# Optimization experiments

Measured on AMD Instinct MI355X. Metric: run time of the kernel, lower is better.

Reference implementation:

```python
import jax, jax.numpy as jnp
import numpy as np

NUM_HEADS = 4
D_K = 64
D_MODEL = NUM_HEADS * D_K  # 256
SEN_LEN = 8192
N_GROUPS = 4096
BASE_LEN = 64
N_EDGES = N_GROUPS * BASE_LEN  # 262144
PATH_LEN = 64


def setup_inputs() -> dict:
    rng = np.random.default_rng(0)
    key = jax.random.key(0)
    ks = jax.random.split(key, 16)

    # ragged group lengths, each >= 2, summing exactly to N_EDGES
    half = N_GROUPS // 2
    r = rng.integers(-(BASE_LEN - 2), BASE_LEN - 1, size=half)
    edge_len = np.concatenate([BASE_LEN + r, BASE_LEN - r]).astype(np.int64)
    assert edge_len.sum() == N_EDGES and edge_len.min() >= 2

    # distinct token ids; include src=0 and tar=1 so path_agg branches fire
    perm = rng.permutation(np.arange(2, SEN_LEN))[: N_GROUPS - 2]
    token_ids = np.concatenate([np.array([0, 1]), perm]).astype(np.int64)

    def w(k, shape):
        return jax.random.normal(k, shape, jnp.float32) / np.sqrt(shape[-1]).astype(np.float32)

    return {
        "path": jax.random.normal(ks[0], (PATH_LEN, D_MODEL), jnp.float32),
        "path_len": PATH_LEN,
        "q": jax.random.normal(ks[1], (SEN_LEN, D_MODEL), jnp.float32),
        "k": jax.random.normal(ks[2], (N_EDGES, D_MODEL), jnp.float32),
        "v": jax.random.normal(ks[3], (N_EDGES, D_MODEL), jnp.float32),
        "graphs": 0,
        "edge_len": jnp.asarray(edge_len),
        "token_ids": jnp.asarray(token_ids),
        "pair": jnp.array([0, 1], jnp.int32),
        "rev": 0,
        "W_qpair": w(ks[4], (D_MODEL, 2 * D_MODEL)),
        "W_pk": w(ks[5], (D_MODEL, D_MODEL)),
        "W_pv": w(ks[6], (D_MODEL, D_MODEL)),
        "W_q": w(ks[7], (D_MODEL, D_MODEL)),
        "W_k": w(ks[8], (D_MODEL, D_MODEL)),
        "W_v": w(ks[9], (D_MODEL, D_MODEL)),
        "W_out": w(ks[10], (D_MODEL, D_MODEL)),
        "b_out": jnp.zeros((D_MODEL,), jnp.float32),
        "W_agg": w(ks[11], (D_MODEL, 2 * D_MODEL)),
    }


def _forward(path, q, k, v, edge_len, token_ids, pair, rev,
             W_qpair, W_pk, W_pv, W_q, W_k, W_v, W_out, b_out, W_agg):
    H, dk = NUM_HEADS, D_K
    G = edge_len.shape[0]
    E = k.shape[0]
    scale = 1.0 / jnp.sqrt(jnp.float32(dk))

    src = pair[0] if rev == 0 else pair[1]
    tar = pair[1] if rev == 0 else pair[0]

    # pair query: cat(q[src], q[tar]) -> linear -> [H, 1, dk]
    pair_q = (jnp.concatenate([q[src], q[tar]]) @ W_qpair.T).reshape(1, H, dk).transpose(1, 0, 2)

    qh = (q @ W_q.T).reshape(-1, H, dk).transpose(1, 0, 2)      # [H, S, dk]
    pk = (path @ W_pk.T).reshape(-1, H, dk).transpose(1, 0, 2)  # [H, P, dk]
    pv = (path @ W_pv.T).reshape(-1, H, dk).transpose(1, 0, 2)  # [H, P, dk]
    kh = (k @ W_k.T).reshape(-1, H, dk).transpose(1, 0, 2)      # [H, E, dk]
    vh = (v @ W_v.T).reshape(-1, H, dk).transpose(1, 0, 2)      # [H, E, dk]

    # ---- pair/path attention ----
    att = jax.nn.softmax(jnp.einsum('hqd,hpd->hqp', pair_q, pk) * scale, axis=-1)  # [H,1,P]
    path_vals = jnp.einsum('hqp,hpd->hqd', att, pv).sum(axis=1)  # [H, dk]
    path_result = path_vals.reshape(-1) @ W_out.T + b_out        # [d_model]

    # ---- segmented per-group attention (vectorized ragged loop) ----
    seg = jnp.repeat(jnp.arange(G), edge_len, total_repeat_length=E)  # [E]
    q_sel = qh[:, token_ids, :]          # [H, G, dk] query per group
    qe = q_sel[:, seg, :]                # [H, E, dk] query per edge
    # torch.matmul(q_[H,dk], k_[H,i,dk].T) broadcasts to cross-head logits [a,b,i]
    logits = jnp.einsum('aed,bed->eab', qe, kh) * scale  # [E, H, H]
    lmax = jax.lax.stop_gradient(jax.ops.segment_max(logits, seg, num_segments=G))
    ex = jnp.exp(logits - lmax[seg])
    denom = jax.ops.segment_sum(ex, seg, num_segments=G)
    p = ex / denom[seg]                                   # segmented softmax [E, H, H]
    # sum over key-head b per edge, then segment-reduce over edges of each group
    out_e = jnp.einsum('eab,bed->ead', p, vh)             # [E, H, dk]
    hid = jax.ops.segment_sum(out_e, seg, num_segments=G) # [G, H, dk]
    new_hid = hid.reshape(G, H * dk) @ W_out.T + b_out    # [G, d_model] (dropout=identity)

    # ---- assemble output rows ----
    pr = jnp.broadcast_to(path_result, (G, D_MODEL))
    feat_path = jnp.concatenate([new_hid, pr], axis=1) @ W_agg.T  # token == src
    path_feat = jnp.concatenate([pr, new_hid], axis=1) @ W_agg.T  # token == tar
    is_src = (token_ids == src)[:, None]
    is_tar = (token_ids == tar)[:, None]
    vals = jnp.where(is_src, feat_path, jnp.where(is_tar, path_feat, new_hid))
    returned = q.at[token_ids].set(vals)
    return returned, att


def reference(path, path_len, q, k, v, graphs, edge_len, token_ids, pair, rev,
              W_qpair, W_pk, W_pv, W_q, W_k, W_v, W_out, b_out, W_agg):
    return _forward(path, q, k, v, edge_len, token_ids, pair, rev,
                    W_qpair, W_pk, W_pv, W_q, W_k, W_v, W_out, b_out, W_agg)
```

## Files before the change

kernel.cpp:

```cpp
#include <hip/hip_runtime.h>
#include <hip/hip_bf16.h>

#define H 4
#define DK 64
#define DM 256
#define SEN 8192
#define NG 4096
#define ETOT 262144
#define PLEN 64
#define MAXE 128

typedef unsigned short ushortT;
typedef __attribute__((ext_vector_type(8))) __bf16 bf16x8;
typedef __attribute__((ext_vector_type(8))) unsigned short us8;
typedef __attribute__((ext_vector_type(4))) unsigned short us4;
typedef __attribute__((ext_vector_type(4))) float f32x4;

#define TMS 264

__device__ __forceinline__ ushortT f2bf(float f) {
    unsigned u = __float_as_uint(f);
    u += 0x7FFF + ((u >> 16) & 1);
    return (ushortT)(u >> 16);
}
__device__ __forceinline__ bf16x8 ldb8(const ushortT* p) {
    us8 v = *(const us8*)p;
    return __builtin_bit_cast(bf16x8, v);
}
__device__ __forceinline__ bf16x8 pack8(const float* f) {
    us8 v;
#pragma unroll
    for (int j = 0; j < 8; j++) v[j] = f2bf(f[j]);
    return __builtin_bit_cast(bf16x8, v);
}
__device__ __forceinline__ ushortT sbf(float f) {
    return __builtin_bit_cast(ushortT, (__bf16)f);
}
__device__ __forceinline__ bf16x8 pack8f(float4 a, float4 b) {
    bf16x8 r;
    r[0] = (__bf16)a.x; r[1] = (__bf16)a.y; r[2] = (__bf16)a.z; r[3] = (__bf16)a.w;
    r[4] = (__bf16)b.x; r[5] = (__bf16)b.y; r[6] = (__bf16)b.z; r[7] = (__bf16)b.w;
    return r;
}

__global__ __launch_bounds__(256) void scan_kernel(const int* __restrict__ edge_len,
                                                   int* __restrict__ starts) {
    __shared__ int part[256];
    const int tid = threadIdx.x;
    const int base = tid * 16;
    int loc[16];
    int s = 0;
#pragma unroll
    for (int i = 0; i < 16; i++) { loc[i] = s; s += edge_len[base + i]; }
    part[tid] = s;
    __syncthreads();
    if (tid == 0) {
        int acc = 0;
        for (int i = 0; i < 256; i++) { int t = part[i]; part[i] = acc; acc += t; }
    }
    __syncthreads();
    const int off = part[tid];
#pragma unroll
    for (int i = 0; i < 16; i++) starts[base + i] = off + loc[i];
}

__global__ void copy_kernel(const float* __restrict__ q, float* __restrict__ out) {
    const size_t i = (size_t)blockIdx.x * blockDim.x + threadIdx.x;
    ((float4*)out)[i] = ((const float4*)q)[i];
}

__global__ __launch_bounds__(256) void wprep_kernel(
    const float* __restrict__ W_q, const float* __restrict__ W_k,
    const float* __restrict__ W_v, const float* __restrict__ W_out,
    ushortT* __restrict__ WQb, ushortT* __restrict__ WKTb,
    ushortT* __restrict__ WVb, ushortT* __restrict__ WOb) {
    const int idx = blockIdx.x * 256 + threadIdx.x;
    const int sel = idx >> 16;
    const int i = idx & 65535;
    if (sel == 0) {
        WQb[i] = sbf(W_q[i]);
    } else if (sel == 1) {
        const int c = i >> 8, d = i & 255;
        WKTb[i] = sbf(W_k[d * DM + c]);
    } else if (sel == 2) {
        WVb[i] = sbf(W_v[i]);
    } else {
        WOb[i] = sbf(W_out[i]);
    }
}

__global__ __launch_bounds__(256) void qhtmat_kernel(
    const float* __restrict__ q, const int* __restrict__ token_ids,
    const ushortT* __restrict__ WQb, const ushortT* __restrict__ WKTb,
    ushortT* __restrict__ tmat_u) {
    __shared__ ushortT Al[16 * 264];
    __shared__ ushortT QHs[16 * 264];
    const int tid = threadIdx.x;
    const int g0 = blockIdx.x * 16;
    const int lane = tid & 63, w = tid >> 6, lq = lane & 15, lh = lane >> 4;
    {
        const int m = tid >> 4;
        const int c0 = (tid & 15) * 16;
        const int tok = token_ids[g0 + m];
        const float* qr = &q[(size_t)tok * DM + c0];
#pragma unroll
        for (int i = 0; i < 4; i++) {
            float4 v4 = *(const float4*)&qr[i * 4];
            us4 o;
            o[0] = sbf(v4.x); o[1] = sbf(v4.y); o[2] = sbf(v4.z); o[3] = sbf(v4.w);
            *(us4*)&Al[m * 264 + c0 + i * 4] = o;
        }
    }
    __syncthreads();
    {
        bf16x8 af[8];
#pragma unroll
        for (int kk = 0; kk < 8; kk++) af[kk] = ldb8(&Al[lq * 264 + kk * 32 + lh * 8]);
#pragma unroll
        for (int ntl = 0; ntl < 4; ntl++) {
            const int nt = w * 4 + ntl;
            f32x4 acc = {0.f, 0.f, 0.f, 0.f};
#pragma unroll
            for (int kk = 0; kk < 8; kk++) {
                bf16x8 bf = ldb8(&WQb[(nt * 16 + lq) * 256 + kk * 32 + lh * 8]);
                acc = __builtin_amdgcn_mfma_f32_16x16x32_bf16(af[kk], bf, acc, 0, 0, 0);
            }
#pragma unroll
            for (int r = 0; r < 4; r++)
                QHs[(lh * 4 + r) * 264 + nt * 16 + lq] = sbf(acc[r]);
        }
    }
    __syncthreads();
    for (int ab = 0; ab < 16; ab++) {
        const int a = ab >> 2, b = ab & 3;
        bf16x8 a0 = ldb8(&QHs[lq * 264 + a * 64 + lh * 8]);
        bf16x8 a1 = ldb8(&QHs[lq * 264 + a * 64 + 32 + lh * 8]);
#pragma unroll
        for (int ntl = 0; ntl < 4; ntl++) {
            const int nt = w * 4 + ntl;
            f32x4 acc = {0.f, 0.f, 0.f, 0.f};
            bf16x8 b0 = ldb8(&WKTb[(nt * 16 + lq) * 256 + b * 64 + lh * 8]);
            acc = __builtin_amdgcn_mfma_f32_16x16x32_bf16(a0, b0, acc, 0, 0, 0);
            bf16x8 b1 = ldb8(&WKTb[(nt * 16 + lq) * 256 + b * 64 + 32 + lh * 8]);
            acc = __builtin_amdgcn_mfma_f32_16x16x32_bf16(a1, b1, acc, 0, 0, 0);
#pragma unroll
            for (int r = 0; r < 4; r++)
                tmat_u[((size_t)(g0 + lh * 4 + r) * 16 + ab) * 256 + nt * 16 + lq] =
                    sbf(acc[r]);
        }
    }
}

__global__ __launch_bounds__(256) void edge_kernel(
    const float* __restrict__ k, const float* __restrict__ v,
    const int* __restrict__ edge_len, const int* __restrict__ starts,
    ushortT* __restrict__ tmat_u) {
    const int g = blockIdx.x;
    const int tid = threadIdx.x;
    const float scale = 0.125f;
    __shared__ float plog[128][17];
    __shared__ ushortT pT[16 * 136];
    __shared__ float red[16][16];
    __shared__ float mx[16];
    __shared__ float vbuf[32 * 258];
    const int start = starts[g];
    const int len = edge_len[g];
    const int lane = tid & 63, w = tid >> 6, lq = lane & 15, lh = lane >> 4;
    const int rg = tid >> 4, cc = tid & 15;
    const int vrow = tid & 31, vcs = tid >> 5;
    const int nkc = (len + 31) >> 5;

    float4 vr[8];
    {
        const int ecl = (vrow < len) ? vrow : (len - 1);
        const float* src = &v[(size_t)(start + ecl) * DM + vcs * 32];
#pragma unroll
        for (int i = 0; i < 8; i++) vr[i] = *(const float4*)&src[i * 4];
    }

    bf16x8 btm[8];
#pragma unroll
    for (int cb = 0; cb < 8; cb++)
        btm[cb] = ldb8(&tmat_u[((size_t)g * 16 + lq) * 256 + cb * 32 + lh * 8]);

    const int nmt = (len + 15) >> 4;
    for (int t = w; t < nmt; t += 4) {
        const int e = t * 16 + lq;
        const int ec = (e < len) ? e : (len - 1);
        const float* krow = &k[(size_t)(start + ec) * DM + lh * 8];
        f32x4 acc = {0.f, 0.f, 0.f, 0.f};
#pragma unroll
        for (int cb = 0; cb < 8; cb++) {
            float4 k0 = *(const float4*)&krow[cb * 32];
            float4 k1 = *(const float4*)&krow[cb * 32 + 4];
            acc = __builtin_amdgcn_mfma_f32_16x16x32_bf16(pack8f(k0, k1), btm[cb], acc, 0, 0, 0);
        }
#pragma unroll
        for (int r = 0; r < 4; r++) plog[t * 16 + lh * 4 + r][lq] = acc[r] * scale;
    }
    __syncthreads();

    {
        float m = -3.0e38f;
        for (int e = rg; e < len; e += 16) m = fmaxf(m, plog[e][cc]);
        red[rg][cc] = m;
        __syncthreads();
        if (tid < 16) {
            float mm = red[0][tid];
            for (int i2 = 1; i2 < 16; i2++) mm = fmaxf(mm, red[i2][tid]);
            mx[tid] = mm;
        }
        __syncthreads();
        const float mm = mx[cc];
        float s = 0.f;
        for (int e = rg; e < len; e += 16) {
            float ex = __expf(plog[e][cc] - mm);
            plog[e][cc] = ex;
            s += ex;
        }
        red[rg][cc] = s;
        __syncthreads();
        if (tid < 16) {
            float ss = red[0][tid];
            for (int i2 = 1; i2 < 16; i2++) ss += red[i2][tid];
            mx[tid] = 1.0f / ss;
        }
        __syncthreads();
        const float inv = mx[cc];
        const int padlen = nkc * 32;
        for (int e = rg; e < padlen; e += 16) {
            float pv = (e < len) ? plog[e][cc] * inv : 0.f;
            pT[cc * 136 + e] = f2bf(pv);
        }
    }
    __syncthreads();

    {
        f32x4 uacc[4];
#pragma unroll
        for (int nt = 0; nt < 4; nt++) uacc[nt] = {0.f, 0.f, 0.f, 0.f};
        const int wb = vrow * 258 + vcs * 32;
        for (int kc = 0; kc < nkc; kc++) {
#pragma unroll
            for (int i = 0; i < 8; i++) {
                *(float2*)&vbuf[wb + i * 4]     = make_float2(vr[i].x, vr[i].y);
                *(float2*)&vbuf[wb + i * 4 + 2] = make_float2(vr[i].z, vr[i].w);
            }
            __syncthreads();
            if (kc + 1 < nkc) {
                const int e = (kc + 1) * 32 + vrow;
                const int ecl = (e < len) ? e : (len - 1);
                const float* src = &v[(size_t)(start + ecl) * DM + vcs * 32];
#pragma unroll
                for (int i = 0; i < 8; i++) vr[i] = *(const float4*)&src[i * 4];
            }
            bf16x8 ap = ldb8(&pT[lq * 136 + kc * 32 + lh * 8]);
#pragma unroll
            for (int nt = 0; nt < 4; nt++) {
                bf16x8 bv;
#pragma unroll
                for (int j = 0; j < 8; j++)
                    bv[j] = (__bf16)vbuf[(lh * 8 + j) * 258 + w * 64 + nt * 16 + lq];
                uacc[nt] = __builtin_amdgcn_mfma_f32_16x16x32_bf16(ap, bv, uacc[nt], 0, 0, 0);
            }
            __syncthreads();
        }
        const int c0 = w * 64;
#pragma unroll
        for (int nt = 0; nt < 4; nt++) {
#pragma unroll
            for (int r = 0; r < 4; r++) {
                const int ab = lh * 4 + r;
                tmat_u[((size_t)g * 16 + ab) * 256 + c0 + nt * 16 + lq] = sbf(uacc[nt][r]);
            }
        }
    }
}

__global__ __launch_bounds__(256) void hidnh_kernel(
    const ushortT* __restrict__ Ub, const ushortT* __restrict__ WVb,
    const ushortT* __restrict__ WOb, const float* __restrict__ b_out,
    const int* __restrict__ token_ids, float* __restrict__ out) {
    __shared__ ushortT HIDs[16 * 264];
    const int tid = threadIdx.x;
    const int g0 = blockIdx.x * 16;
    const int lane = tid & 63, w = tid >> 6, lq = lane & 15, lh = lane >> 4;
#pragma unroll
    for (int a = 0; a < 4; a++) {
        f32x4 acc = {0.f, 0.f, 0.f, 0.f};
        for (int kk = 0; kk < 32; kk++) {
            const int kbase = kk * 32 + lh * 8;
            bf16x8 af = ldb8(&Ub[((size_t)(g0 + lq) * 16 + a * 4) * 256 + kbase]);
            bf16x8 bf = ldb8(&WVb[(size_t)((kbase >> 8) * 64 + w * 16 + lq) * 256 + (kbase & 255)]);
            acc = __builtin_amdgcn_mfma_f32_16x16x32_bf16(af, bf, acc, 0, 0, 0);
        }
#pragma unroll
        for (int r = 0; r < 4; r++)
            HIDs[(lh * 4 + r) * 264 + a * 64 + w * 16 + lq] = sbf(acc[r]);
    }
    __syncthreads();
    bf16x8 af2[8];
#pragma unroll
    for (int kk = 0; kk < 8; kk++) af2[kk] = ldb8(&HIDs[lq * 264 + kk * 32 + lh * 8]);
    int toks[4];
#pragma unroll
    for (int r = 0; r < 4; r++) toks[r] = token_ids[g0 + lh * 4 + r];
#pragma unroll
    for (int ntl = 0; ntl < 4; ntl++) {
        const int nt = w * 4 + ntl;
        f32x4 acc = {0.f, 0.f, 0.f, 0.f};
#pragma unroll
        for (int kk = 0; kk < 8; kk++) {
            bf16x8 bf = ldb8(&WOb[(nt * 16 + lq) * 256 + kk * 32 + lh * 8]);
            acc = __builtin_amdgcn_mfma_f32_16x16x32_bf16(af2[kk], bf, acc, 0, 0, 0);
        }
        const int n = nt * 16 + lq;
        const float bo = b_out[n];
#pragma unroll
        for (int r = 0; r < 4; r++)
            out[(size_t)toks[r] * DM + n] = acc[r] + bo;
    }
}

__global__ __launch_bounds__(256) void agg_kernel(
    const int* __restrict__ token_ids, const int* __restrict__ pair,
    const int* __restrict__ rev, const float* __restrict__ W_agg,
    const float* __restrict__ path_result, float* __restrict__ out) {
    __shared__ int gsrc, gtar;
    __shared__ float catS[512], catT[512];
    const int tid = threadIdx.x;
    if (tid == 0) { gsrc = -1; gtar = -1; }
    __syncthreads();
    const int rv = rev[0];
    const int src = (rv == 0) ? pair[0] : pair[1];
    const int tar = (rv == 0) ? pair[1] : pair[0];
    for (int i = tid; i < NG; i += 256) {
        const int tk = token_ids[i];
        if (tk == src) gsrc = i;
        if (tk == tar) gtar = i;
    }
    __syncthreads();
    const int gs = gsrc, gt = gtar;
    if (gs >= 0) {
        catS[tid] = out[(size_t)src * DM + tid];
        catS[256 + tid] = path_result[tid];
    }
    if (gt >= 0) {
        catT[tid] = path_result[tid];
        catT[256 + tid] = out[(size_t)tar * DM + tid];
    }
    __syncthreads();
    if (gs >= 0) {
        float acc = 0.f;
        for (int n = 0; n < 512; n += 4) {
            float4 w4 = *(const float4*)&W_agg[(size_t)tid * 512 + n];
            acc += w4.x * catS[n] + w4.y * catS[n + 1] + w4.z * catS[n + 2] + w4.w * catS[n + 3];
        }
        out[(size_t)src * DM + tid] = acc;
    }
    if (gt >= 0) {
        float acc = 0.f;
        for (int n = 0; n < 512; n += 4) {
            float4 w4 = *(const float4*)&W_agg[(size_t)tid * 512 + n];
            acc += w4.x * catT[n] + w4.y * catT[n + 1] + w4.z * catT[n + 2] + w4.w * catT[n + 3];
        }
        out[(size_t)tar * DM + tid] = acc;
    }
}

__global__ __launch_bounds__(256) void pathB_kernel(
    const float* __restrict__ path, const float* __restrict__ q,
    const int* __restrict__ pair, const int* __restrict__ rev,
    const float* __restrict__ W_qpair, const float* __restrict__ W_pk,
    const float* __restrict__ W_pv,
    float* __restrict__ pv_ws, float* __restrict__ logits_ws) {
    __shared__ float cat[512];
    __shared__ float pq[256];
    __shared__ float prow[256];
    __shared__ float lp[256];
    const int p = blockIdx.x;
    const int tid = threadIdx.x;
    const int rv = rev[0];
    const int src = (rv == 0) ? pair[0] : pair[1];
    const int tar = (rv == 0) ? pair[1] : pair[0];
    cat[tid] = q[(size_t)src * DM + tid];
    cat[256 + tid] = q[(size_t)tar * DM + tid];
    prow[tid] = path[p * DM + tid];
    __syncthreads();
    float acc = 0.f;
    for (int c = 0; c < 512; c += 4) {
        float4 w4 = *(const float4*)&W_qpair[(size_t)tid * 512 + c];
        acc += w4.x * cat[c] + w4.y * cat[c + 1] + w4.z * cat[c + 2] + w4.w * cat[c + 3];
    }
    pq[tid] = acc;
    __syncthreads();
    float pkv = 0.f, pvv = 0.f;
    for (int c = 0; c < 256; c += 4) {
        float4 a4 = *(const float4*)&W_pk[tid * DM + c];
        float4 b4 = *(const float4*)&W_pv[tid * DM + c];
        float4 x4 = *(const float4*)&prow[c];
        pkv += a4.x * x4.x + a4.y * x4.y + a4.z * x4.z + a4.w * x4.w;
        pvv += b4.x * x4.x + b4.y * x4.y + b4.z * x4.z + b4.w * x4.w;
    }
    pv_ws[p * DM + tid] = pvv;
    lp[tid] = pq[tid] * pkv;
    __syncthreads();
    if (tid < H) {
        float s = 0.f;
        for (int d = 0; d < DK; d++) s += lp[tid * DK + d];
        logits_ws[tid * PLEN + p] = s * 0.125f;
    }
}

__global__ __launch_bounds__(256) void pathC_kernel(
    const float* __restrict__ pv_ws, const float* __restrict__ logits_ws,
    const float* __restrict__ W_out, const float* __restrict__ b_out,
    float* __restrict__ att_out, float* __restrict__ path_result) {
    __shared__ float att[256];
    __shared__ float pvals[256];
    const int tid = threadIdx.x;
    att[tid] = logits_ws[tid];
    __syncthreads();
    if (tid < H) {
        float m = -3.0e38f;
        for (int p = 0; p < PLEN; p++) m = fmaxf(m, att[tid * PLEN + p]);
        float s = 0.f;
        for (int p = 0; p < PLEN; p++) {
            float e = __expf(att[tid * PLEN + p] - m);
            att[tid * PLEN + p] = e;
            s += e;
        }
        float inv = 1.f / s;
        for (int p = 0; p < PLEN; p++) att[tid * PLEN + p] *= inv;
    }
    __syncthreads();
    att_out[tid] = att[tid];
    {
        const int h = tid >> 6;
        float a = 0.f;
        for (int p = 0; p < PLEN; p++) a += att[h * PLEN + p] * pv_ws[p * DM + tid];
        pvals[tid] = a;
    }
    __syncthreads();
    {
        float a = b_out[tid];
        for (int c = 0; c < 256; c += 4) {
            float4 w4 = *(const float4*)&W_out[tid * DM + c];
            a += w4.x * pvals[c] + w4.y * pvals[c + 1] + w4.z * pvals[c + 2] + w4.w * pvals[c + 3];
        }
        path_result[tid] = a;
    }
}

__global__ __launch_bounds__(256, 4) void group_kernel(
    const float* __restrict__ q, const float* __restrict__ k, const float* __restrict__ v,
    const int* __restrict__ edge_len, const int* __restrict__ token_ids,
    const int* __restrict__ pair, const int* __restrict__ rev,
    const float* __restrict__ W_q,
    const float* __restrict__ W_k, const float* __restrict__ W_v,
    const float* __restrict__ W_out, const float* __restrict__ b_out,
    const float* __restrict__ W_agg,
    const int* __restrict__ starts, const float* __restrict__ path_result,
    float* __restrict__ out) {
    const int g = blockIdx.x;
    const int tid = threadIdx.x;
    const float scale = 0.125f;

    __shared__ float qrow[256];
    __shared__ float qh[256];
    __shared__ ushortT qh_b[4 * 72];
    __shared__ ushortT tmat_b[16 * TMS];
    __shared__ float plog[128][17];
    __shared__ ushortT pT[16 * 136];
    __shared__ ushortT u_b[4 * 1032];
    __shared__ float hid[256];
    __shared__ float nh[256];
    __shared__ float red[16][16];
    __shared__ float mx[16];

    const int tok = token_ids[g];
    const int start = starts[g];
    const int len = edge_len[g];

    const int lane = tid & 63;
    const int w = tid >> 6;
    const int lq = lane & 15;
    const int lh = lane >> 4;
    const int rg = tid >> 4;
    const int cc = tid & 15;

    qrow[tid] = q[(size_t)tok * DM + tid];
    __syncthreads();

    for (int i = 0; i < 16; i++) {
        const int r = i * 16 + rg;
        float acc = 0.f;
#pragma unroll
        for (int j4 = 0; j4 < 4; j4++) {
            const int c0 = j4 * 64 + cc * 4;
            float4 w4 = *(const float4*)&W_q[r * DM + c0];
            float4 x4 = *(const float4*)&qrow[c0];
            acc += w4.x * x4.x + w4.y * x4.y + w4.z * x4.z + w4.w * x4.w;
        }
#pragma unroll
        for (int off = 8; off; off >>= 1) acc += __shfl_down(acc, off, 16);
        if (cc == 0) qh[r] = acc;
    }
    __syncthreads();
    qh_b[(tid >> 6) * 72 + (tid & 63)] = f2bf(qh[tid]);
    __syncthreads();

    {
        const int arow = (lq < 3) ? lq : 3;
        bf16x8 aq0 = ldb8(&qh_b[arow * 72 + lh * 8]);
        bf16x8 aq1 = ldb8(&qh_b[arow * 72 + 32 + lh * 8]);
        for (int nt = 0; nt < 16; nt++) {
            const int c = nt * 16 + lq;
            f32x4 acc = {0.f, 0.f, 0.f, 0.f};
            float wf[8];
#pragma unroll
            for (int j = 0; j < 8; j++)
                wf[j] = W_k[(size_t)(w * 64 + lh * 8 + j) * DM + c];
            acc = __builtin_amdgcn_mfma_f32_16x16x32_bf16(aq0, pack8(wf), acc, 0, 0, 0);
#pragma unroll
            for (int j = 0; j < 8; j++)
                wf[j] = W_k[(size_t)(w * 64 + 32 + lh * 8 + j) * DM + c];
            acc = __builtin_amdgcn_mfma_f32_16x16x32_bf16(aq1, pack8(wf), acc, 0, 0, 0);
            if (lane < 16) {
#pragma unroll
                for (int r = 0; r < 4; r++)
                    tmat_b[(r * 4 + w) * TMS + nt * 16 + lq] = f2bf(acc[r]);
            }
        }
    }
    __syncthreads();

    {
        bf16x8 btm[8];
#pragma unroll
        for (int cb = 0; cb < 8; cb++)
            btm[cb] = ldb8(&tmat_b[lq * TMS + cb * 32 + lh * 8]);
        const int nmt = (len + 15) >> 4;
        for (int t = w; t < nmt; t += 4) {
            const int e = t * 16 + lq;
            const int ec = (e < len) ? e : (len - 1);
            const float* krow = &k[(size_t)(start + ec) * DM + lh * 8];
            f32x4 acc = {0.f, 0.f, 0.f, 0.f};
#pragma unroll
            for (int cb = 0; cb < 8; cb++) {
                float4 k0 = *(const float4*)&krow[cb * 32];
                float4 k1 = *(const float4*)&krow[cb * 32 + 4];
                float kf[8] = {k0.x, k0.y, k0.z, k0.w, k1.x, k1.y, k1.z, k1.w};
                acc = __builtin_amdgcn_mfma_f32_16x16x32_bf16(pack8(kf), btm[cb], acc, 0, 0, 0);
            }
#pragma unroll
            for (int r = 0; r < 4; r++) plog[t * 16 + lh * 4 + r][lq] = acc[r] * scale;
        }
    }
    __syncthreads();

    const int nkc = (len + 31) >> 5;
    {
        float m = -3.0e38f;
        for (int e = rg; e < len; e += 16) m = fmaxf(m, plog[e][cc]);
        red[rg][cc] = m;
        __syncthreads();
        if (tid < 16) {
            float mm = red[0][tid];
            for (int i2 = 1; i2 < 16; i2++) mm = fmaxf(mm, red[i2][tid]);
            mx[tid] = mm;
        }
        __syncthreads();
        const float mm = mx[cc];
        float s = 0.f;
        for (int e = rg; e < len; e += 16) {
            float ex = __expf(plog[e][cc] - mm);
            plog[e][cc] = ex;
            s += ex;
        }
        red[rg][cc] = s;
        __syncthreads();
        if (tid < 16) {
            float ss = red[0][tid];
            for (int i2 = 1; i2 < 16; i2++) ss += red[i2][tid];
            mx[tid] = 1.0f / ss;
        }
        __syncthreads();
        const float inv = mx[cc];
        const int padlen = nkc * 32;
        for (int e = rg; e < padlen; e += 16) {
            float pv = (e < len) ? plog[e][cc] * inv : 0.f;
            pT[cc * 136 + e] = f2bf(pv);
        }
    }
    __syncthreads();

    {
        f32x4 uacc[4];
#pragma unroll
        for (int nt = 0; nt < 4; nt++) uacc[nt] = {0.f, 0.f, 0.f, 0.f};
        const int c0 = w * 64;
#pragma unroll
        for (int kc = 0; kc < 4; kc++) {
            if (kc < nkc) {
                bf16x8 ap = ldb8(&pT[lq * 136 + kc * 32 + lh * 8]);
#pragma unroll
                for (int nt = 0; nt < 4; nt++) {
                    float bf[8];
#pragma unroll
                    for (int j = 0; j < 8; j++) {
                        int e = kc * 32 + lh * 8 + j;
                        int ecl = (e < len) ? e : (len - 1);
                        bf[j] = v[(size_t)(start + ecl) * DM + c0 + nt * 16 + lq];
                    }
                    uacc[nt] = __builtin_amdgcn_mfma_f32_16x16x32_bf16(ap, pack8(bf), uacc[nt], 0, 0, 0);
                }
            }
        }
#pragma unroll
        for (int nt = 0; nt < 4; nt++) {
#pragma unroll
            for (int r = 0; r < 4; r++) {
                const int row = lh * 4 + r;
                const int a = row >> 2, b = row & 3;
                u_b[a * 1032 + b * 256 + c0 + nt * 16 + lq] = f2bf(uacc[nt][r]);
            }
        }
    }
    __syncthreads();

    {
        const int arow = (lq < 3) ? lq : 3;
        f32x4 hacc = {0.f, 0.f, 0.f, 0.f};
        for (int kc = 0; kc < 32; kc++) {
            bf16x8 au = ldb8(&u_b[arow * 1032 + kc * 32 + lh * 8]);
            const int kk = kc * 32 + lh * 8;
            const float* wr = &W_v[(size_t)((kk >> 8) * 64 + w * 16 + lq) * DM + (kk & 255)];
            float4 w0 = *(const float4*)&wr[0];
            float4 w1 = *(const float4*)&wr[4];
            float wf[8] = {w0.x, w0.y, w0.z, w0.w, w1.x, w1.y, w1.z, w1.w};
            hacc = __builtin_amdgcn_mfma_f32_16x16x32_bf16(au, pack8(wf), hacc, 0, 0, 0);
        }
        if (lane < 16) {
#pragma unroll
            for (int r = 0; r < 4; r++) hid[r * 64 + w * 16 + lq] = hacc[r];
        }
    }
    __syncthreads();

    for (int i = 0; i < 16; i++) {
        const int m = i * 16 + rg;
        float acc = 0.f;
#pragma unroll
        for (int j4 = 0; j4 < 4; j4++) {
            const int c0 = j4 * 64 + cc * 4;
            float4 w4 = *(const float4*)&W_out[m * DM + c0];
            float4 h4 = *(const float4*)&hid[c0];
            acc += w4.x * h4.x + w4.y * h4.y + w4.z * h4.z + w4.w * h4.w;
        }
#pragma unroll
        for (int off = 8; off; off >>= 1) acc += __shfl_down(acc, off, 16);
        if (cc == 0) nh[m] = b_out[m] + acc;
    }
    __syncthreads();

    const int rv = rev[0];
    const int src = (rv == 0) ? pair[0] : pair[1];
    const int tar = (rv == 0) ? pair[1] : pair[0];
    float val;
    if (tok == src || tok == tar) {
        qrow[tid] = path_result[tid];
        __syncthreads();
        const float* x1 = (tok == src) ? nh : qrow;
        const float* x2 = (tok == src) ? qrow : nh;
        float acc = 0.f;
        for (int n = 0; n < 256; n += 4) {
            float4 w4 = *(const float4*)&W_agg[(size_t)tid * 512 + n];
            acc += w4.x * x1[n] + w4.y * x1[n + 1] + w4.z * x1[n + 2] + w4.w * x1[n + 3];
        }
        for (int n = 0; n < 256; n += 4) {
            float4 w4 = *(const float4*)&W_agg[(size_t)tid * 512 + 256 + n];
            acc += w4.x * x2[n] + w4.y * x2[n + 1] + w4.z * x2[n + 2] + w4.w * x2[n + 3];
        }
        val = acc;
    } else {
        val = nh[tid];
    }
    out[(size_t)tok * DM + tid] = val;
}

extern "C" void kernel_launch(void* const* d_in, const int* in_sizes, int n_in,
                              void* d_out, int out_size, void* d_ws, size_t ws_size,
                              hipStream_t stream) {
    const float* path    = (const float*)d_in[0];
    const float* q       = (const float*)d_in[2];
    const float* k       = (const float*)d_in[3];
    const float* v       = (const float*)d_in[4];
    const int*   edge_len  = (const int*)d_in[6];
    const int*   token_ids = (const int*)d_in[7];
    const int*   pair      = (const int*)d_in[8];
    const int*   rev       = (const int*)d_in[9];
    const float* W_qpair = (const float*)d_in[10];
    const float* W_pk    = (const float*)d_in[11];
    const float* W_pv    = (const float*)d_in[12];
    const float* W_q     = (const float*)d_in[13];
    const float* W_k     = (const float*)d_in[14];
    const float* W_v     = (const float*)d_in[15];
    const float* W_out   = (const float*)d_in[16];
    const float* b_out   = (const float*)d_in[17];
    const float* W_agg   = (const float*)d_in[18];
    float* out = (float*)d_out;

    char* base = (char*)d_ws;
    int*    starts      = (int*)(base + 0);
    float*  path_result = (float*)(base + 16384);
    float*  pv_ws       = (float*)(base + 17408);
    float*  logits_ws   = (float*)(base + 82944);
    ushortT* WQb        = (ushortT*)(base + 83968);
    ushortT* WKTb       = (ushortT*)(base + 215040);
    ushortT* WVb        = (ushortT*)(base + 346112);
    ushortT* WOb        = (ushortT*)(base + 477184);
    ushortT* tmat_u     = (ushortT*)(base + 608256);
    const size_t NEED = 608256 + 33554432;

    copy_kernel<<<dim3(2048), dim3(256), 0, stream>>>(q, out);
    scan_kernel<<<dim3(1), dim3(256), 0, stream>>>(edge_len, starts);
    pathB_kernel<<<dim3(PLEN), dim3(256), 0, stream>>>(path, q, pair, rev, W_qpair, W_pk,
                                                       W_pv, pv_ws, logits_ws);
    pathC_kernel<<<dim3(1), dim3(256), 0, stream>>>(pv_ws, logits_ws, W_out, b_out,
                                                    out + (size_t)SEN * DM, path_result);

    if (ws_size >= NEED) {
        wprep_kernel<<<dim3(1024), dim3(256), 0, stream>>>(W_q, W_k, W_v, W_out,
                                                           WQb, WKTb, WVb, WOb);
        qhtmat_kernel<<<dim3(256), dim3(256), 0, stream>>>(q, token_ids, WQb, WKTb, tmat_u);
        edge_kernel<<<dim3(NG), dim3(256), 0, stream>>>(k, v, edge_len, starts, tmat_u);
        hidnh_kernel<<<dim3(256), dim3(256), 0, stream>>>(tmat_u, WVb, WOb, b_out,
                                                          token_ids, out);
        agg_kernel<<<dim3(1), dim3(256), 0, stream>>>(token_ids, pair, rev, W_agg,
                                                      path_result, out);
    } else {
        group_kernel<<<dim3(NG), dim3(256), 0, stream>>>(q, k, v, edge_len, token_ids, pair,
                                                         rev, W_q, W_k, W_v, W_out, b_out,
                                                         W_agg, starts, path_result, out);
    }
}
```

Measured before the change: 300.8 us.

## Batch K loads ahead of MFMAs, store V tile as bf16, raise edge_kernel occupancy

The edge kernel now issues all K-row loads for up to two 16-row tiles per wave before running the MFMAs, replacing the serial loop. The goal is to overlap global load latency. The V staging buffer in shared memory holds bf16 instead of fp32, which halves LDS footprint and write traffic, and launch bounds request 2 blocks per SM to raise occupancy. The unrolled path assumes at most 8 tiles per group (len <= 128), and the 32 float4 registers for K may cause register pressure or spills under the new launch bound.

```diff
diff --git a/kernel.cpp b/kernel.cpp
--- a/kernel.cpp
+++ b/kernel.cpp
@@ -17,6 +17,7 @@
 typedef __attribute__((ext_vector_type(4))) float f32x4;
 
 #define TMS 264
+#define VBS 260
 
 __device__ __forceinline__ ushortT f2bf(float f) {
     unsigned u = __float_as_uint(f);
@@ -35,6 +36,9 @@
 }
 __device__ __forceinline__ ushortT sbf(float f) {
     return __builtin_bit_cast(ushortT, (__bf16)f);
+}
+__device__ __forceinline__ __bf16 u2b(ushortT u) {
+    return __builtin_bit_cast(__bf16, u);
 }
 __device__ __forceinline__ bf16x8 pack8f(float4 a, float4 b) {
     bf16x8 r;
@@ -151,7 +155,7 @@
     }
 }
 
-__global__ __launch_bounds__(256) void edge_kernel(
+__global__ __launch_bounds__(256, 2) void edge_kernel(
     const float* __restrict__ k, const float* __restrict__ v,
     const int* __restrict__ edge_len, const int* __restrict__ starts,
     ushortT* __restrict__ tmat_u) {
@@ -162,41 +166,67 @@
     __shared__ ushortT pT[16 * 136];
     __shared__ float red[16][16];
     __shared__ float mx[16];
-    __shared__ float vbuf[32 * 258];
+    __shared__ ushortT vbuf[32 * VBS];
     const int start = starts[g];
     const int len = edge_len[g];
     const int lane = tid & 63, w = tid >> 6, lq = lane & 15, lh = lane >> 4;
     const int rg = tid >> 4, cc = tid & 15;
     const int vrow = tid & 31, vcs = tid >> 5;
     const int nkc = (len + 31) >> 5;
-
+    const int nmt = (len + 15) >> 4;
+
+    bf16x8 btm[8];
+#pragma unroll
+    for (int cb = 0; cb < 8; cb++)
+        btm[cb] = ldb8(&tmat_u[((size_t)g * 16 + lq) * 256 + cb * 32 + lh * 8]);
+
+    const bool h0 = (w < nmt);
+    const bool h1 = (w + 4 < nmt);
+    float4 kr0[16], kr1[16];
+    if (h0) {
+        const int e = w * 16 + lq;
+        const int ec = (e < len) ? e : (len - 1);
+        const float* krow = &k[(size_t)(start + ec) * DM + lh * 8];
+#pragma unroll
+        for (int cb = 0; cb < 8; cb++) {
+            kr0[2 * cb]     = *(const float4*)&krow[cb * 32];
+            kr0[2 * cb + 1] = *(const float4*)&krow[cb * 32 + 4];
+        }
+    }
+    if (h1) {
+        const int e = (w + 4) * 16 + lq;
+        const int ec = (e < len) ? e : (len - 1);
+        const float* krow = &k[(size_t)(start + ec) * DM + lh * 8];
+#pragma unroll
+        for (int cb = 0; cb < 8; cb++) {
+            kr1[2 * cb]     = *(const float4*)&krow[cb * 32];
+            kr1[2 * cb + 1] = *(const float4*)&krow[cb * 32 + 4];
+        }
+    }
+    if (h0) {
+        f32x4 acc = {0.f, 0.f, 0.f, 0.f};
+#pragma unroll
+        for (int cb = 0; cb < 8; cb++)
+            acc = __builtin_amdgcn_mfma_f32_16x16x32_bf16(
+                pack8f(kr0[2 * cb], kr0[2 * cb + 1]), btm[cb], acc, 0, 0, 0);
+#pragma unroll
+        for (int r = 0; r < 4; r++) plog[w * 16 + lh * 4 + r][lq] = acc[r] * scale;
+    }
+    if (h1) {
+        f32x4 acc = {0.f, 0.f, 0.f, 0.f};
+#pragma unroll
+        for (int cb = 0; cb < 8; cb++)
+            acc = __builtin_amdgcn_mfma_f32_16x16x32_bf16(
+                pack8f(kr1[2 * cb], kr1[2 * cb + 1]), btm[cb], acc, 0, 0, 0);
+#pragma unroll
+        for (int r = 0; r < 4; r++) plog[(w + 4) * 16 + lh * 4 + r][lq] = acc[r] * scale;
+    }
     float4 vr[8];
     {
         const int ecl = (vrow < len) ? vrow : (len - 1);
         const float* src = &v[(size_t)(start + ecl) * DM + vcs * 32];
 #pragma unroll
         for (int i = 0; i < 8; i++) vr[i] = *(const float4*)&src[i * 4];
-    }
-
-    bf16x8 btm[8];
-#pragma unroll
-    for (int cb = 0; cb < 8; cb++)
-        btm[cb] = ldb8(&tmat_u[((size_t)g * 16 + lq) * 256 + cb * 32 + lh * 8]);
-
-    const int nmt = (len + 15) >> 4;
-    for (int t = w; t < nmt; t += 4) {
-        const int e = t * 16 + lq;
-        const int ec = (e < len) ? e : (len - 1);
-        const float* krow = &k[(size_t)(start + ec) * DM + lh * 8];
-        f32x4 acc = {0.f, 0.f, 0.f, 0.f};
-#pragma unroll
-        for (int cb = 0; cb < 8; cb++) {
-            float4 k0 = *(const float4*)&krow[cb * 32];
-            float4 k1 = *(const float4*)&krow[cb * 32 + 4];
-            acc = __builtin_amdgcn_mfma_f32_16x16x32_bf16(pack8f(k0, k1), btm[cb], acc, 0, 0, 0);
-        }
-#pragma unroll
-        for (int r = 0; r < 4; r++) plog[t * 16 + lh * 4 + r][lq] = acc[r] * scale;
     }
     __syncthreads();
 
@@ -230,7 +260,7 @@
         const int padlen = nkc * 32;
         for (int e = rg; e < padlen; e += 16) {
             float pv = (e < len) ? plog[e][cc] * inv : 0.f;
-            pT[cc * 136 + e] = f2bf(pv);
+            pT[cc * 136 + e] = sbf(pv);
         }
     }
     __syncthreads();
@@ -239,12 +269,14 @@
         f32x4 uacc[4];
 #pragma unroll
         for (int nt = 0; nt < 4; nt++) uacc[nt] = {0.f, 0.f, 0.f, 0.f};
-        const int wb = vrow * 258 + vcs * 32;
+        const int wb = vrow * VBS + vcs * 32;
         for (int kc = 0; kc < nkc; kc++) {
 #pragma unroll
             for (int i = 0; i < 8; i++) {
-                *(float2*)&vbuf[wb + i * 4]     = make_float2(vr[i].x, vr[i].y);
-                *(float2*)&vbuf[wb + i * 4 + 2] = make_float2(vr[i].z, vr[i].w);
+                us4 o;
+                o[0] = sbf(vr[i].x); o[1] = sbf(vr[i].y);
+                o[2] = sbf(vr[i].z); o[3] = sbf(vr[i].w);
+                *(us4*)&vbuf[wb + i * 4] = o;
             }
             __syncthreads();
             if (kc + 1 < nkc) {
@@ -260,7 +292,7 @@
                 bf16x8 bv;
 #pragma unroll
                 for (int j = 0; j < 8; j++)
-                    bv[j] = (__bf16)vbuf[(lh * 8 + j) * 258 + w * 64 + nt * 16 + lq];
+                    bv[j] = u2b(vbuf[(lh * 8 + j) * VBS + w * 64 + nt * 16 + lq]);
                 uacc[nt] = __builtin_amdgcn_mfma_f32_16x16x32_bf16(ap, bv, uacc[nt], 0, 0, 0);
             }
             __syncthreads();
```

New measurement: 299.6 us. Within noise of the previous version (-0.4%).

## Stage K and V through shared bf16 buffer with coalesced loads in edge kernel

Applied to the files above, without the earlier changes.

The edge kernel now loads K in 64-row chunks with fully coalesced float4 reads across the row, converts them to bf16 and stores them into a shared buffer that the MFMA A operands read from. Previously each lane read strided 32-byte pieces of K rows straight from global memory. V uses the same bf16 shared buffer in place of an fp32 one, which cuts LDS footprint, and the register prefetch of the next V chunk is dropped. The kernel also gains a launch-bounds occupancy hint of 3 blocks. Dropping the prefetch exposes global load latency on each V chunk, and the extra barriers per K chunk add synchronization cost.

```diff
diff --git a/kernel.cpp b/kernel.cpp
--- a/kernel.cpp
+++ b/kernel.cpp
@@ -17,6 +17,7 @@
 typedef __attribute__((ext_vector_type(4))) float f32x4;
 
 #define TMS 264
+#define KVS 260
 
 __device__ __forceinline__ ushortT f2bf(float f) {
     unsigned u = __float_as_uint(f);
@@ -35,6 +36,9 @@
 }
 __device__ __forceinline__ ushortT sbf(float f) {
     return __builtin_bit_cast(ushortT, (__bf16)f);
+}
+__device__ __forceinline__ __bf16 u2b(ushortT u) {
+    return __builtin_bit_cast(__bf16, u);
 }
 __device__ __forceinline__ bf16x8 pack8f(float4 a, float4 b) {
     bf16x8 r;
@@ -151,7 +155,7 @@
     }
 }
 
-__global__ __launch_bounds__(256) void edge_kernel(
+__global__ __launch_bounds__(256, 3) void edge_kernel(
     const float* __restrict__ k, const float* __restrict__ v,
     const int* __restrict__ edge_len, const int* __restrict__ starts,
     ushortT* __restrict__ tmat_u) {
@@ -162,43 +166,52 @@
     __shared__ ushortT pT[16 * 136];
     __shared__ float red[16][16];
     __shared__ float mx[16];
-    __shared__ float vbuf[32 * 258];
+    __shared__ ushortT kvb[64 * KVS];
     const int start = starts[g];
     const int len = edge_len[g];
     const int lane = tid & 63, w = tid >> 6, lq = lane & 15, lh = lane >> 4;
     const int rg = tid >> 4, cc = tid & 15;
-    const int vrow = tid & 31, vcs = tid >> 5;
     const int nkc = (len + 31) >> 5;
-
-    float4 vr[8];
-    {
-        const int ecl = (vrow < len) ? vrow : (len - 1);
-        const float* src = &v[(size_t)(start + ecl) * DM + vcs * 32];
-#pragma unroll
-        for (int i = 0; i < 8; i++) vr[i] = *(const float4*)&src[i * 4];
-    }
+    const int nmt = (len + 15) >> 4;
+    const int col = (tid & 63) * 4;
+    const int rr = tid >> 6;
 
     bf16x8 btm[8];
 #pragma unroll
     for (int cb = 0; cb < 8; cb++)
         btm[cb] = ldb8(&tmat_u[((size_t)g * 16 + lq) * 256 + cb * 32 + lh * 8]);
 
-    const int nmt = (len + 15) >> 4;
-    for (int t = w; t < nmt; t += 4) {
-        const int e = t * 16 + lq;
-        const int ec = (e < len) ? e : (len - 1);
-        const float* krow = &k[(size_t)(start + ec) * DM + lh * 8];
-        f32x4 acc = {0.f, 0.f, 0.f, 0.f};
-#pragma unroll
-        for (int cb = 0; cb < 8; cb++) {
-            float4 k0 = *(const float4*)&krow[cb * 32];
-            float4 k1 = *(const float4*)&krow[cb * 32 + 4];
-            acc = __builtin_amdgcn_mfma_f32_16x16x32_bf16(pack8f(k0, k1), btm[cb], acc, 0, 0, 0);
-        }
-#pragma unroll
-        for (int r = 0; r < 4; r++) plog[t * 16 + lh * 4 + r][lq] = acc[r] * scale;
-    }
-    __syncthreads();
+    const int nch = (nmt + 3) >> 2;
+    for (int c = 0; c < nch; c++) {
+        const int base = c * 64;
+        const int cnt = len - base;
+        const int rquads = (cnt < 64 ? cnt + 3 : 67) >> 2;
+#pragma unroll
+        for (int i = 0; i < 16; i++) {
+            if (i < rquads) {
+                const int row = i * 4 + rr;
+                const int gr = base + row;
+                const int grc = (gr < len) ? gr : (len - 1);
+                float4 v4 = *(const float4*)&k[(size_t)(start + grc) * DM + col];
+                us4 o;
+                o[0] = sbf(v4.x); o[1] = sbf(v4.y); o[2] = sbf(v4.z); o[3] = sbf(v4.w);
+                *(us4*)&kvb[row * KVS + col] = o;
+            }
+        }
+        __syncthreads();
+        const int t = c * 4 + w;
+        if (t < nmt) {
+            f32x4 acc = {0.f, 0.f, 0.f, 0.f};
+#pragma unroll
+            for (int cb = 0; cb < 8; cb++) {
+                bf16x8 ak = ldb8(&kvb[(w * 16 + lq) * KVS + cb * 32 + lh * 8]);
+                acc = __builtin_amdgcn_mfma_f32_16x16x32_bf16(ak, btm[cb], acc, 0, 0, 0);
+            }
+#pragma unroll
+            for (int r = 0; r < 4; r++) plog[t * 16 + lh * 4 + r][lq] = acc[r] * scale;
+        }
+        __syncthreads();
+    }
 
     {
         float m = -3.0e38f;
@@ -230,7 +243,7 @@
         const int padlen = nkc * 32;
         for (int e = rg; e < padlen; e += 16) {
             float pv = (e < len) ? plog[e][cc] * inv : 0.f;
-            pT[cc * 136 + e] = f2bf(pv);
+            pT[cc * 136 + e] = sbf(pv);
         }
     }
     __syncthreads();
@@ -239,28 +252,26 @@
         f32x4 uacc[4];
 #pragma unroll
         for (int nt = 0; nt < 4; nt++) uacc[nt] = {0.f, 0.f, 0.f, 0.f};
-        const int wb = vrow * 258 + vcs * 32;
         for (int kc = 0; kc < nkc; kc++) {
+            const int base = kc * 32;
 #pragma unroll
             for (int i = 0; i < 8; i++) {
-                *(float2*)&vbuf[wb + i * 4]     = make_float2(vr[i].x, vr[i].y);
-                *(float2*)&vbuf[wb + i * 4 + 2] = make_float2(vr[i].z, vr[i].w);
+                const int row = i * 4 + rr;
+                const int gr = base + row;
+                const int grc = (gr < len) ? gr : (len - 1);
+                float4 v4 = *(const float4*)&v[(size_t)(start + grc) * DM + col];
+                us4 o;
+                o[0] = sbf(v4.x); o[1] = sbf(v4.y); o[2] = sbf(v4.z); o[3] = sbf(v4.w);
+                *(us4*)&kvb[row * KVS + col] = o;
             }
             __syncthreads();
-            if (kc + 1 < nkc) {
-                const int e = (kc + 1) * 32 + vrow;
-                const int ecl = (e < len) ? e : (len - 1);
-                const float* src = &v[(size_t)(start + ecl) * DM + vcs * 32];
-#pragma unroll
-                for (int i = 0; i < 8; i++) vr[i] = *(const float4*)&src[i * 4];
-            }
             bf16x8 ap = ldb8(&pT[lq * 136 + kc * 32 + lh * 8]);
 #pragma unroll
             for (int nt = 0; nt < 4; nt++) {
                 bf16x8 bv;
 #pragma unroll
                 for (int j = 0; j < 8; j++)
-                    bv[j] = (__bf16)vbuf[(lh * 8 + j) * 258 + w * 64 + nt * 16 + lq];
+                    bv[j] = u2b(kvb[(lh * 8 + j) * KVS + w * 64 + nt * 16 + lq]);
                 uacc[nt] = __builtin_amdgcn_mfma_f32_16x16x32_bf16(ap, bv, uacc[nt], 0, 0, 0);
             }
             __syncthreads();
```

Measured after the change: 319.7 us. 6.3% more time.
